# Performance work log

Hardware: AMD Instinct MI355X
Metric: run time of the kernel (lower is better)

The kernel has to match this reference:

```python
import jax, jax.numpy as jnp
import numpy as np

B, S, D, N_OPS = 16, 8192, 128, 4


def setup_inputs() -> dict:
    key = jax.random.key(0)
    k1, k2, k3 = jax.random.split(key, 3)
    x = jax.random.normal(k1, (B, S, D), dtype=jnp.float32)
    # candidate op parameters: 4 Linear(D, D) layers, stacked
    W = jax.random.normal(k2, (N_OPS, D, D), dtype=jnp.float32) * (1.0 / np.sqrt(D))
    b = jax.random.normal(k3, (N_OPS, D), dtype=jnp.float32) * 0.01
    # one-hot path selector buffer: weights[0] = 1.0 (as in MixModule.__init__)
    weights = jnp.zeros((N_OPS,), dtype=jnp.float32).at[0].set(1.0)
    return {"x": x, "W": W, "b": b, "weights": weights}


def reference(x, W, b, weights):
    # Faithful to the torch loop: compute EVERY candidate op(x), then the
    # weighted (one-hot) sum. outs: [B, S, n_ops, D]
    outs = jnp.einsum("bsd,ofd->bsof", x, W) + b[None, None, :, :]
    y = jnp.einsum("bsof,o->bsf", outs, weights)
    return y
```

## Files before the change

kernel.cpp:

```cpp
#include <hip/hip_runtime.h>
#include <hip/hip_bf16.h>

#define D 128
#define NOPS 4
#define BS_STRIDE 136

typedef __attribute__((ext_vector_type(8))) short short8;
typedef __attribute__((ext_vector_type(4))) float float4_t;

__global__ void combine_kernel(const float* __restrict__ W,
                               const float* __restrict__ b,
                               const float* __restrict__ wts,
                               __hip_bfloat16* __restrict__ Wc,
                               float* __restrict__ bc) {
    int idx = blockIdx.x * blockDim.x + threadIdx.x;
    float w0 = wts[0], w1 = wts[1], w2 = wts[2], w3 = wts[3];
    if (idx < D * D) {
        float v = w0 * W[idx] + w1 * W[D * D + idx]
                + w2 * W[2 * D * D + idx] + w3 * W[3 * D * D + idx];
        Wc[idx] = __float2bfloat16(v);
    }
    if (idx < D) {
        bc[idx] = w0 * b[idx] + w1 * b[D + idx] + w2 * b[2 * D + idx] + w3 * b[3 * D + idx];
    }
}

__device__ inline short8 cvt8_bf16(float4_t a, float4_t b) {
    union { short8 s; __hip_bfloat16 h[8]; } u;
    u.h[0] = __float2bfloat16(a[0]);
    u.h[1] = __float2bfloat16(a[1]);
    u.h[2] = __float2bfloat16(a[2]);
    u.h[3] = __float2bfloat16(a[3]);
    u.h[4] = __float2bfloat16(b[0]);
    u.h[5] = __float2bfloat16(b[1]);
    u.h[6] = __float2bfloat16(b[2]);
    u.h[7] = __float2bfloat16(b[3]);
    return u.s;
}

__global__ __launch_bounds__(256) void gemm_kernel(const float* __restrict__ x,
                                                   const __hip_bfloat16* __restrict__ Wc,
                                                   const float* __restrict__ bc,
                                                   float* __restrict__ y,
                                                   int M) {
    __shared__ __align__(16) __hip_bfloat16 Bs[D * BS_STRIDE];

    const int tid  = threadIdx.x;
    const int lane = tid & 63;
    const int wave = tid >> 6;

    #pragma unroll
    for (int i = 0; i < 8; i++) {
        int c  = i * 256 + tid;
        int n  = c >> 4;
        int ko = (c & 15) << 3;
        short8 v = *(const short8*)((const short*)Wc + n * D + ko);
        *(short8*)((short*)Bs + n * BS_STRIDE + ko) = v;
    }
    __syncthreads();

    const int m0 = (blockIdx.x * 4 + wave) * 16;
    if (m0 >= M) return;

    const int row  = lane & 15;
    const int quad = lane >> 4;

    float4_t acc[8];
    #pragma unroll
    for (int i = 0; i < 8; i++) acc[i] = (float4_t)(0.f);

    #pragma unroll
    for (int ks = 0; ks < 4; ks++) {
        const float* ap = x + (size_t)(m0 + row) * D + ks * 32 + quad * 8;
        float4_t a0 = *(const float4_t*)ap;
        float4_t a1 = *(const float4_t*)(ap + 4);
        short8 afrag = cvt8_bf16(a0, a1);

        const short* bp = (const short*)Bs + ks * 32 + quad * 8;
        #pragma unroll
        for (int nt = 0; nt < 8; nt++) {
            short8 bfrag = *(const short8*)(bp + (nt * 16 + row) * BS_STRIDE);
            acc[nt] = __builtin_amdgcn_mfma_f32_16x16x32_bf16(afrag, bfrag, acc[nt], 0, 0, 0);
        }
    }

    #pragma unroll
    for (int nt = 0; nt < 8; nt++) {
        int col = nt * 16 + row;
        float bias = bc[col];
        #pragma unroll
        for (int r = 0; r < 4; r++) {
            int m = m0 + quad * 4 + r;
            y[(size_t)m * D + col] = acc[nt][r] + bias;
        }
    }
}

extern "C" void kernel_launch(void* const* d_in, const int* in_sizes, int n_in,
                              void* d_out, int out_size, void* d_ws, size_t ws_size,
                              hipStream_t stream) {
    const float* x   = (const float*)d_in[0];
    const float* W   = (const float*)d_in[1];
    const float* b   = (const float*)d_in[2];
    const float* wts = (const float*)d_in[3];
    float* y = (float*)d_out;

    __hip_bfloat16* Wc = (__hip_bfloat16*)d_ws;
    float* bc = (float*)((char*)d_ws + D * D * sizeof(__hip_bfloat16));

    combine_kernel<<<(D * D + 255) / 256, 256, 0, stream>>>(W, b, wts, Wc, bc);

    const int M = in_sizes[0] / D;
    gemm_kernel<<<M / 64, 256, 0, stream>>>(x, Wc, bc, y, M);
}
```

Baseline: 126.1 us.

## Swap MFMA operands for vectorized stores, process two slabs per block, nontemporal IO

The MFMA operands are swapped so that each lane's accumulator holds four consecutive output columns of a single row. This lets the epilogue write float4 vectors instead of scattered scalar stores. Each block now handles two 64-row slabs, which amortizes the shared-memory load of the weights, and all x loads are issued before the MFMAs. Loads and stores use nontemporal hints, bias is preloaded as vectors, and launch bounds request 4 blocks per CU; these may raise register pressure or hurt if the nontemporal hints bypass useful caching.

```diff
diff --git a/kernel.cpp b/kernel.cpp
--- a/kernel.cpp
+++ b/kernel.cpp
@@ -4,6 +4,7 @@
 #define D 128
 #define NOPS 4
 #define BS_STRIDE 136
+#define NSLAB 2
 
 typedef __attribute__((ext_vector_type(8))) short short8;
 typedef __attribute__((ext_vector_type(4))) float float4_t;
@@ -38,11 +39,11 @@
     return u.s;
 }
 
-__global__ __launch_bounds__(256) void gemm_kernel(const float* __restrict__ x,
-                                                   const __hip_bfloat16* __restrict__ Wc,
-                                                   const float* __restrict__ bc,
-                                                   float* __restrict__ y,
-                                                   int M) {
+__global__ __launch_bounds__(256, 4) void gemm_kernel(const float* __restrict__ x,
+                                                      const __hip_bfloat16* __restrict__ Wc,
+                                                      const float* __restrict__ bc,
+                                                      float* __restrict__ y,
+                                                      int M) {
     __shared__ __align__(16) __hip_bfloat16 Bs[D * BS_STRIDE];
 
     const int tid  = threadIdx.x;
@@ -57,41 +58,56 @@
         short8 v = *(const short8*)((const short*)Wc + n * D + ko);
         *(short8*)((short*)Bs + n * BS_STRIDE + ko) = v;
     }
-    __syncthreads();
-
-    const int m0 = (blockIdx.x * 4 + wave) * 16;
-    if (m0 >= M) return;
 
     const int row  = lane & 15;
     const int quad = lane >> 4;
 
-    float4_t acc[8];
+    float4_t bias[8];
     #pragma unroll
-    for (int i = 0; i < 8; i++) acc[i] = (float4_t)(0.f);
+    for (int ft = 0; ft < 8; ft++)
+        bias[ft] = *(const float4_t*)(bc + ft * 16 + quad * 4);
+
+    __syncthreads();
+
+    if (blockIdx.x * (64 * NSLAB) >= M) return;
+    const int mbase = blockIdx.x * (64 * NSLAB) + wave * 16 + row;
 
     #pragma unroll
-    for (int ks = 0; ks < 4; ks++) {
-        const float* ap = x + (size_t)(m0 + row) * D + ks * 32 + quad * 8;
-        float4_t a0 = *(const float4_t*)ap;
-        float4_t a1 = *(const float4_t*)(ap + 4);
-        short8 afrag = cvt8_bf16(a0, a1);
+    for (int s = 0; s < NSLAB; s++) {
+        const int m = mbase + s * 64;
 
-        const short* bp = (const short*)Bs + ks * 32 + quad * 8;
+        const float* xp = x + (size_t)m * D + quad * 8;
+        short8 xf[4];
         #pragma unroll
-        for (int nt = 0; nt < 8; nt++) {
-            short8 bfrag = *(const short8*)(bp + (nt * 16 + row) * BS_STRIDE);
-            acc[nt] = __builtin_amdgcn_mfma_f32_16x16x32_bf16(afrag, bfrag, acc[nt], 0, 0, 0);
+        for (int ks = 0; ks < 4; ks++) {
+            float4_t a0 = __builtin_nontemporal_load((const float4_t*)(xp + ks * 32));
+            float4_t a1 = __builtin_nontemporal_load((const float4_t*)(xp + ks * 32 + 4));
+            xf[ks] = cvt8_bf16(a0, a1);
         }
-    }
 
-    #pragma unroll
-    for (int nt = 0; nt < 8; nt++) {
-        int col = nt * 16 + row;
-        float bias = bc[col];
+        float4_t acc[8];
         #pragma unroll
-        for (int r = 0; r < 4; r++) {
-            int m = m0 + quad * 4 + r;
-            y[(size_t)m * D + col] = acc[nt][r] + bias;
+        for (int i = 0; i < 8; i++) acc[i] = (float4_t)(0.f);
+
+        #pragma unroll
+        for (int ks = 0; ks < 4; ks++) {
+            const short* bp = (const short*)Bs + ks * 32 + quad * 8;
+            #pragma unroll
+            for (int ft = 0; ft < 8; ft++) {
+                short8 wfrag = *(const short8*)(bp + (ft * 16 + row) * BS_STRIDE);
+                acc[ft] = __builtin_amdgcn_mfma_f32_16x16x32_bf16(wfrag, xf[ks], acc[ft], 0, 0, 0);
+            }
+        }
+
+        float* yp = y + (size_t)m * D + quad * 4;
+        #pragma unroll
+        for (int ft = 0; ft < 8; ft++) {
+            float4_t out;
+            out[0] = acc[ft][0] + bias[ft][0];
+            out[1] = acc[ft][1] + bias[ft][1];
+            out[2] = acc[ft][2] + bias[ft][2];
+            out[3] = acc[ft][3] + bias[ft][3];
+            __builtin_nontemporal_store(out, (float4_t*)(yp + ft * 16));
         }
     }
 }
@@ -111,5 +127,5 @@
     combine_kernel<<<(D * D + 255) / 256, 256, 0, stream>>>(W, b, wts, Wc, bc);
 
     const int M = in_sizes[0] / D;
-    gemm_kernel<<<M / 64, 256, 0, stream>>>(x, Wc, bc, y, M);
+    gemm_kernel<<<M / (64 * NSLAB), 256, 0, stream>>>(x, Wc, bc, y, M);
 }
```

Result: slower. 132.6 us (+5.2%).

## Pipeline x tiles through LDS with async global_load_lds triple buffering

Applied to the files above, without the earlier changes.

Each block now handles 256 rows as eight 32-row tiles. Each tile is staged into a triple-buffered, XOR-swizzled LDS area with global_load_lds, and waits are tuned by vmcnt so the next loads overlap the MFMA work. The combined weight is held in registers as MFMA fragments, so W is no longer staged through LDS. Output is written as float4 stores transposed via swapped MFMA operands. The aim is to hide memory latency on this bandwidth-bound GEMM, at the cost of fewer blocks and hand-counted waitcnts that are fragile.

```diff
diff --git a/kernel.cpp b/kernel.cpp
--- a/kernel.cpp
+++ b/kernel.cpp
@@ -2,11 +2,17 @@
 #include <hip/hip_bf16.h>
 
 #define D 128
-#define NOPS 4
-#define BS_STRIDE 136
+#define TILE_ROWS 32
+#define TPB 8
+#define NBUF 3
+#define TILE_BYTES (TILE_ROWS * D * 4)
+#define ROWS_PER_BLOCK (TILE_ROWS * TPB)
 
 typedef __attribute__((ext_vector_type(8))) short short8;
 typedef __attribute__((ext_vector_type(4))) float float4_t;
+
+typedef const __attribute__((address_space(1))) void g_void;
+typedef __attribute__((address_space(3))) void l_void;
 
 __global__ void combine_kernel(const float* __restrict__ W,
                                const float* __restrict__ b,
@@ -25,7 +31,7 @@
     }
 }
 
-__device__ inline short8 cvt8_bf16(float4_t a, float4_t b) {
+__device__ __forceinline__ short8 cvt8_bf16(float4_t a, float4_t b) {
     union { short8 s; __hip_bfloat16 h[8]; } u;
     u.h[0] = __float2bfloat16(a[0]);
     u.h[1] = __float2bfloat16(a[1]);
@@ -38,62 +44,115 @@
     return u.s;
 }
 
-__global__ __launch_bounds__(256) void gemm_kernel(const float* __restrict__ x,
-                                                   const __hip_bfloat16* __restrict__ Wc,
-                                                   const float* __restrict__ bc,
-                                                   float* __restrict__ y,
-                                                   int M) {
-    __shared__ __align__(16) __hip_bfloat16 Bs[D * BS_STRIDE];
+template<int N>
+__device__ __forceinline__ void vwait() {
+    asm volatile("s_waitcnt vmcnt(%0)" :: "i"(N) : "memory");
+    __builtin_amdgcn_sched_barrier(0);
+}
+
+__device__ __forceinline__ void stage_tile(const float* xg, char* lds, int tid) {
+    #pragma unroll
+    for (int g = 0; g < 4; g++) {
+        int R  = g * 8 + (tid >> 5);
+        int sl = tid & 31;
+        const char* src = (const char*)xg + R * 512 + ((sl ^ (R & 7)) << 4);
+        char* dst = lds + g * 4096 + (tid >> 6) * 1024;
+        __builtin_amdgcn_global_load_lds((g_void*)src, (l_void*)dst, 16, 0, 0);
+    }
+}
+
+__global__ __launch_bounds__(256, 1) void gemm_kernel(const float* __restrict__ x,
+                                                      const __hip_bfloat16* __restrict__ Wc,
+                                                      const float* __restrict__ bc,
+                                                      float* __restrict__ y, int M) {
+    __shared__ __align__(16) char Bs[NBUF * TILE_BYTES];
 
     const int tid  = threadIdx.x;
     const int lane = tid & 63;
     const int wave = tid >> 6;
+    const int r    = lane & 15;
+    const int quad = lane >> 4;
+    const int hb   = wave & 1;
+    const int ch   = wave >> 1;
 
+    const int row0 = blockIdx.x * ROWS_PER_BLOCK;
+    if (row0 >= M) return;
+    const float* xblk = x + (size_t)row0 * D;
+
+    short8 wf[4][4];
     #pragma unroll
-    for (int i = 0; i < 8; i++) {
-        int c  = i * 256 + tid;
-        int n  = c >> 4;
-        int ko = (c & 15) << 3;
-        short8 v = *(const short8*)((const short*)Wc + n * D + ko);
-        *(short8*)((short*)Bs + n * BS_STRIDE + ko) = v;
-    }
-    __syncthreads();
+    for (int f = 0; f < 4; f++)
+        #pragma unroll
+        for (int ks = 0; ks < 4; ks++)
+            wf[f][ks] = *(const short8*)((const short*)Wc
+                          + (ch * 64 + f * 16 + r) * D + ks * 32 + quad * 8);
 
-    const int m0 = (blockIdx.x * 4 + wave) * 16;
-    if (m0 >= M) return;
+    float4_t bias[4];
+    #pragma unroll
+    for (int f = 0; f < 4; f++)
+        bias[f] = *(const float4_t*)(bc + ch * 64 + f * 16 + quad * 4);
 
-    const int row  = lane & 15;
-    const int quad = lane >> 4;
+    int dsoff[4][2];
+    #pragma unroll
+    for (int ks = 0; ks < 4; ks++)
+        #pragma unroll
+        for (int h = 0; h < 2; h++)
+            dsoff[ks][h] = (hb * 16 + r) * 512
+                         + (((ks * 8 + quad * 2 + h) ^ (r & 7)) << 4);
 
-    float4_t acc[8];
-    #pragma unroll
-    for (int i = 0; i < 8; i++) acc[i] = (float4_t)(0.f);
+    stage_tile(xblk,                Bs,              tid);
+    stage_tile(xblk + TILE_ROWS * D, Bs + TILE_BYTES, tid);
 
-    #pragma unroll
-    for (int ks = 0; ks < 4; ks++) {
-        const float* ap = x + (size_t)(m0 + row) * D + ks * 32 + quad * 8;
-        float4_t a0 = *(const float4_t*)ap;
-        float4_t a1 = *(const float4_t*)(ap + 4);
-        short8 afrag = cvt8_bf16(a0, a1);
-
-        const short* bp = (const short*)Bs + ks * 32 + quad * 8;
-        #pragma unroll
-        for (int nt = 0; nt < 8; nt++) {
-            short8 bfrag = *(const short8*)(bp + (nt * 16 + row) * BS_STRIDE);
-            acc[nt] = __builtin_amdgcn_mfma_f32_16x16x32_bf16(afrag, bfrag, acc[nt], 0, 0, 0);
-        }
+#define TILE_STEP(T, NW)                                                        \
+    {                                                                           \
+        if ((T) + 2 < TPB)                                                      \
+            stage_tile(xblk + ((T) + 2) * TILE_ROWS * D,                        \
+                       Bs + (((T) + 2) % NBUF) * TILE_BYTES, tid);              \
+        vwait<NW>();                                                            \
+        __builtin_amdgcn_s_barrier();                                           \
+        const char* buf = Bs + ((T) % NBUF) * TILE_BYTES;                       \
+        short8 xf[4];                                                           \
+        _Pragma("unroll")                                                       \
+        for (int ks = 0; ks < 4; ks++) {                                        \
+            float4_t a0 = *(const float4_t*)(buf + dsoff[ks][0]);               \
+            float4_t a1 = *(const float4_t*)(buf + dsoff[ks][1]);               \
+            xf[ks] = cvt8_bf16(a0, a1);                                         \
+        }                                                                       \
+        asm volatile("s_waitcnt lgkmcnt(0)" ::: "memory");                      \
+        __builtin_amdgcn_sched_barrier(0);                                      \
+        __builtin_amdgcn_s_barrier();     \
+        float4_t acc[4];                                                        \
+        _Pragma("unroll")                                                       \
+        for (int f = 0; f < 4; f++) acc[f] = (float4_t)(0.f);                   \
+        _Pragma("unroll")                                                       \
+        for (int ks = 0; ks < 4; ks++) {                                        \
+            _Pragma("unroll")                                                   \
+            for (int f = 0; f < 4; f++)                                         \
+                acc[f] = __builtin_amdgcn_mfma_f32_16x16x32_bf16(               \
+                    wf[f][ks], xf[ks], acc[f], 0, 0, 0);                        \
+        }                                                                       \
+        float* yp = y + (size_t)(row0 + (T) * TILE_ROWS + hb * 16 + r) * D      \
+                      + ch * 64 + quad * 4;                                     \
+        _Pragma("unroll")                                                       \
+        for (int f = 0; f < 4; f++) {                                           \
+            float4_t out;                                                       \
+            out[0] = acc[f][0] + bias[f][0];                                    \
+            out[1] = acc[f][1] + bias[f][1];                                    \
+            out[2] = acc[f][2] + bias[f][2];                                    \
+            out[3] = acc[f][3] + bias[f][3];                                    \
+            *(float4_t*)(yp + f * 16) = out;                                    \
+        }                                                                       \
     }
 
-    #pragma unroll
-    for (int nt = 0; nt < 8; nt++) {
-        int col = nt * 16 + row;
-        float bias = bc[col];
-        #pragma unroll
-        for (int r = 0; r < 4; r++) {
-            int m = m0 + quad * 4 + r;
-            y[(size_t)m * D + col] = acc[nt][r] + bias;
-        }
-    }
+    TILE_STEP(0, 8)
+    TILE_STEP(1, 12)
+    TILE_STEP(2, 16)
+    TILE_STEP(3, 16)
+    TILE_STEP(4, 16)
+    TILE_STEP(5, 16)
+    TILE_STEP(6, 12)
+    TILE_STEP(7, 8)
+#undef TILE_STEP
 }
 
 extern "C" void kernel_launch(void* const* d_in, const int* in_sizes, int n_in,
@@ -111,5 +170,5 @@
     combine_kernel<<<(D * D + 255) / 256, 256, 0, stream>>>(W, b, wts, Wc, bc);
 
     const int M = in_sizes[0] / D;
-    gemm_kernel<<<M / 64, 256, 0, stream>>>(x, Wc, bc, y, M);
+    gemm_kernel<<<M / ROWS_PER_BLOCK, 256, 0, stream>>>(x, Wc, bc, y, M);
 }
```

New measurement: 121.1 us. 1.04x faster.

## Keep weights in registers and double-buffer x tiles via async global-to-LDS loads

Applied to the files above, without the earlier changes.

Each wave now holds the combined bf16 weight fragments in registers instead of staging them in shared memory. It processes four 16-row tiles, loading x through global_load_lds into swizzled, double-buffered LDS so the next tile's load overlaps the current MFMA work. MFMA operands are swapped so each lane writes float4 rows, giving vectorized output stores, and bias is folded into the accumulator init. The change raises register pressure (128 VGPRs for weights) and depends on hand-placed waitcnt and sched_barrier ordering being correct.

```diff
diff --git a/kernel.cpp b/kernel.cpp
--- a/kernel.cpp
+++ b/kernel.cpp
@@ -2,11 +2,14 @@
 #include <hip/hip_bf16.h>
 
 #define D 128
-#define NOPS 4
-#define BS_STRIDE 136
+#define TPW 4
+#define ROWS_PER_BLOCK 256
 
 typedef __attribute__((ext_vector_type(8))) short short8;
 typedef __attribute__((ext_vector_type(4))) float float4_t;
+
+typedef const __attribute__((address_space(1))) void g_void;
+typedef __attribute__((address_space(3))) void l_void;
 
 __global__ void combine_kernel(const float* __restrict__ W,
                                const float* __restrict__ b,
@@ -25,7 +28,7 @@
     }
 }
 
-__device__ inline short8 cvt8_bf16(float4_t a, float4_t b) {
+__device__ __forceinline__ short8 cvt8_bf16(float4_t a, float4_t b) {
     union { short8 s; __hip_bfloat16 h[8]; } u;
     u.h[0] = __float2bfloat16(a[0]);
     u.h[1] = __float2bfloat16(a[1]);
@@ -38,62 +41,96 @@
     return u.s;
 }
 
-__global__ __launch_bounds__(256) void gemm_kernel(const float* __restrict__ x,
-                                                   const __hip_bfloat16* __restrict__ Wc,
-                                                   const float* __restrict__ bc,
-                                                   float* __restrict__ y,
-                                                   int M) {
-    __shared__ __align__(16) __hip_bfloat16 Bs[D * BS_STRIDE];
+__global__ __launch_bounds__(256, 2) void gemm_kernel(const float* __restrict__ x,
+                                                      const __hip_bfloat16* __restrict__ Wc,
+                                                      const float* __restrict__ bc,
+                                                      float* __restrict__ y, int M) {
+    __shared__ __align__(16) char Bs[4 * 2 * 8192];
 
     const int tid  = threadIdx.x;
     const int lane = tid & 63;
     const int wave = tid >> 6;
+    const int r    = lane & 15;
+    const int quad = lane >> 4;
+    const int half = lane >> 5;
+    const int p    = lane & 31;
 
+    char* wbase = Bs + wave * 16384;
+
+    const int row0 = blockIdx.x * ROWS_PER_BLOCK + wave * 64;
+    if (row0 >= M) return;
+    const float* xw = x + (size_t)row0 * D;
+
+    short8 wf[8][4];
     #pragma unroll
-    for (int i = 0; i < 8; i++) {
-        int c  = i * 256 + tid;
-        int n  = c >> 4;
-        int ko = (c & 15) << 3;
-        short8 v = *(const short8*)((const short*)Wc + n * D + ko);
-        *(short8*)((short*)Bs + n * BS_STRIDE + ko) = v;
-    }
-    __syncthreads();
+    for (int f = 0; f < 8; f++)
+        #pragma unroll
+        for (int ks = 0; ks < 4; ks++)
+            wf[f][ks] = *(const short8*)((const short*)Wc
+                          + (f * 16 + r) * D + ks * 32 + quad * 8);
 
-    const int m0 = (blockIdx.x * 4 + wave) * 16;
-    if (m0 >= M) return;
+    float4_t bias[8];
+    #pragma unroll
+    for (int f = 0; f < 8; f++)
+        bias[f] = *(const float4_t*)(bc + f * 16 + quad * 4);
 
-    const int row  = lane & 15;
-    const int quad = lane >> 4;
+    int roff[4][2];
+    #pragma unroll
+    for (int ks = 0; ks < 4; ks++)
+        #pragma unroll
+        for (int h = 0; h < 2; h++)
+            roff[ks][h] = r * 512 + (((ks * 8 + quad * 2 + h) ^ (r & 7)) << 4);
 
-    float4_t acc[8];
-    #pragma unroll
-    for (int i = 0; i < 8; i++) acc[i] = (float4_t)(0.f);
-
-    #pragma unroll
-    for (int ks = 0; ks < 4; ks++) {
-        const float* ap = x + (size_t)(m0 + row) * D + ks * 32 + quad * 8;
-        float4_t a0 = *(const float4_t*)ap;
-        float4_t a1 = *(const float4_t*)(ap + 4);
-        short8 afrag = cvt8_bf16(a0, a1);
-
-        const short* bp = (const short*)Bs + ks * 32 + quad * 8;
-        #pragma unroll
-        for (int nt = 0; nt < 8; nt++) {
-            short8 bfrag = *(const short8*)(bp + (nt * 16 + row) * BS_STRIDE);
-            acc[nt] = __builtin_amdgcn_mfma_f32_16x16x32_bf16(afrag, bfrag, acc[nt], 0, 0, 0);
-        }
+#define STAGE(t) {                                                              \
+        const char* tb = (const char*)(xw + (t) * 16 * D);                      \
+        char* db = wbase + ((t) & 1) * 8192;                                    \
+        _Pragma("unroll")                                                       \
+        for (int g = 0; g < 8; g++) {                                           \
+            int sr = g * 2 + half;                                              \
+            const char* src = tb + sr * 512 + ((p ^ (sr & 7)) << 4);            \
+            __builtin_amdgcn_global_load_lds((g_void*)src,                      \
+                                             (l_void*)(db + g * 1024), 16, 0, 0); \
+        }                                                                       \
     }
 
-    #pragma unroll
-    for (int nt = 0; nt < 8; nt++) {
-        int col = nt * 16 + row;
-        float bias = bc[col];
-        #pragma unroll
-        for (int r = 0; r < 4; r++) {
-            int m = m0 + quad * 4 + r;
-            y[(size_t)m * D + col] = acc[nt][r] + bias;
-        }
+    STAGE(0)
+
+#define STEP(T, NW) {                                                           \
+        asm volatile("s_waitcnt vmcnt(%0)" :: "i"(NW) : "memory");              \
+        __builtin_amdgcn_sched_barrier(0);                                      \
+        const char* buf = wbase + ((T) & 1) * 8192;                             \
+        short8 xf[4];                                                           \
+        _Pragma("unroll")                                                       \
+        for (int ks = 0; ks < 4; ks++) {                                        \
+            float4_t a0 = *(const float4_t*)(buf + roff[ks][0]);                \
+            float4_t a1 = *(const float4_t*)(buf + roff[ks][1]);                \
+            xf[ks] = cvt8_bf16(a0, a1);                                         \
+        }                                                                       \
+        asm volatile("s_waitcnt lgkmcnt(0)" ::: "memory");                      \
+        __builtin_amdgcn_sched_barrier(0);                                      \
+        if ((T) + 1 < TPW) STAGE((T) + 1)                                       \
+        float4_t acc[8];                                                        \
+        _Pragma("unroll")                                                       \
+        for (int f = 0; f < 8; f++) acc[f] = bias[f];                           \
+        _Pragma("unroll")                                                       \
+        for (int ks = 0; ks < 4; ks++) {                                        \
+            _Pragma("unroll")                                                   \
+            for (int f = 0; f < 8; f++)                                         \
+                acc[f] = __builtin_amdgcn_mfma_f32_16x16x32_bf16(               \
+                    wf[f][ks], xf[ks], acc[f], 0, 0, 0);                        \
+        }                                                                       \
+        float* yp = y + (size_t)(row0 + (T) * 16 + r) * D + quad * 4;           \
+        _Pragma("unroll")                                                       \
+        for (int f = 0; f < 8; f++)                                             \
+            *(float4_t*)(yp + f * 16) = acc[f];                                 \
     }
+
+    STEP(0, 0)
+    STEP(1, 8)
+    STEP(2, 8)
+    STEP(3, 8)
+#undef STEP
+#undef STAGE
 }
 
 extern "C" void kernel_launch(void* const* d_in, const int* in_sizes, int n_in,
@@ -111,5 +148,5 @@
     combine_kernel<<<(D * D + 255) / 256, 256, 0, stream>>>(W, b, wts, Wc, bc);
 
     const int M = in_sizes[0] / D;
-    gemm_kernel<<<M / 64, 256, 0, stream>>>(x, Wc, bc, y, M);
+    gemm_kernel<<<M / ROWS_PER_BLOCK, 256, 0, stream>>>(x, Wc, bc, y, M);
 }
```

New measurement: 126.3 us. Within noise of the previous version (+0.2%).
